# Performance work log

Measured on AMD Instinct MI355X. Metric: run time of the kernel, lower is better.

The kernel has to match this reference:

```python
import jax, jax.numpy as jnp
import numpy as np

B, S, H, NH = 1, 4096, 768, 12
D = H // NH  # per-head dim = 64


def setup_inputs() -> dict:
    key = jax.random.key(0)
    ks = jax.random.split(key, 10)
    p = 0.02  # param scale
    return {
        "x": jax.random.normal(ks[0], (B, S, H), jnp.float32),
        "Wq": jax.random.normal(ks[1], (H, H), jnp.float32) * p,
        "bq": jax.random.normal(ks[2], (H,), jnp.float32) * p,
        "Wk": jax.random.normal(ks[3], (H, H), jnp.float32) * p,
        "bk": jax.random.normal(ks[4], (H,), jnp.float32) * p,
        "Wv": jax.random.normal(ks[5], (H, H), jnp.float32) * p,
        "bv": jax.random.normal(ks[6], (H,), jnp.float32) * p,
        "Wo": jax.random.normal(ks[7], (H, H), jnp.float32) * p,
        "bo": jax.random.normal(ks[8], (H,), jnp.float32) * p,
        "attn_mask": jax.random.randint(ks[9], (B, 1, 1, S), 0, 2).astype(bool),
    }


def _split_heads(t):
    # [B, S, H] -> [B, NH, S, D]
    return t.reshape(B, S, NH, D).transpose(0, 2, 1, 3)


def reference(x, Wq, bq, Wk, bk, Wv, bv, Wo, bo, attn_mask):
    q = _split_heads(x @ Wq.T + bq)
    k = _split_heads(x @ Wk.T + bk)
    v = _split_heads(x @ Wv.T + bv)
    scores = jnp.einsum('bhqd,bhkd->bhqk', q, k) / np.sqrt(D).astype(np.float32)
    scores = jnp.where(attn_mask, jnp.float32(-1e9), scores)
    attn = jax.nn.softmax(scores, axis=-1)
    ctx = jnp.einsum('bhqk,bhkd->bhqd', attn, v)
    ctx = ctx.transpose(0, 2, 1, 3).reshape(B, S, H)  # merge heads
    return ctx @ Wo.T + bo
```

## Files before the change

kernel.cpp:

```cpp
#include <hip/hip_runtime.h>
#include <stdint.h>

#define S_LEN 4096
#define HDIM  768
#define NHEAD 12
#define DHEAD 64

typedef _Float16 f16;
typedef __attribute__((ext_vector_type(8))) _Float16 f16x8;
typedef __attribute__((ext_vector_type(4))) _Float16 f16x4;
typedef __attribute__((ext_vector_type(4))) float   f32x4;

typedef __attribute__((address_space(1))) void gv_t;
typedef __attribute__((address_space(3))) void lv_t;

__device__ __forceinline__ void async_copy16(const void* g, void* l) {
  __builtin_amdgcn_global_load_lds((gv_t*)g, (lv_t*)l, 16, 0, 0);
}

__device__ __forceinline__ float fast_exp2(float x) {
#if __has_builtin(__builtin_amdgcn_exp2f)
  return __builtin_amdgcn_exp2f(x);
#else
  return exp2f(x);
#endif
}

__device__ __forceinline__ int swz4(int row) { return (row ^ (row >> 2)) & 3; }

constexpr size_t OFF_META = 0;
constexpr size_t OFF_POS  = 256;
constexpr size_t OFF_XB   = 65536;
constexpr size_t SZ_XB    = (size_t)S_LEN * HDIM * 2;
constexpr size_t OFF_WQKV = OFF_XB + SZ_XB;
constexpr size_t SZ_WQKV  = (size_t)3 * HDIM * HDIM * 2;
constexpr size_t OFF_WO   = OFF_WQKV + SZ_WQKV;
constexpr size_t SZ_WO    = (size_t)HDIM * HDIM * 2;
constexpr size_t OFF_Q    = OFF_WO + SZ_WO;
constexpr size_t SZ_HD    = (size_t)NHEAD * S_LEN * DHEAD * 2;
constexpr size_t OFF_K    = OFF_Q + SZ_HD;
constexpr size_t OFF_VT   = OFF_K + SZ_HD;
constexpr size_t OFF_CTX  = OFF_VT + SZ_HD;
constexpr size_t SZ_CTX   = (size_t)S_LEN * HDIM * 2;
constexpr size_t OFF_PO   = OFF_CTX + SZ_CTX;
constexpr size_t SZ_PO    = (size_t)2 * NHEAD * S_LEN * DHEAD * 2;
constexpr size_t OFF_PL   = OFF_PO + SZ_PO;

__global__ __launch_bounds__(256) void k_cvt5(const float* __restrict__ x,
                                              const float* __restrict__ wq,
                                              const float* __restrict__ wk,
                                              const float* __restrict__ wv,
                                              const float* __restrict__ wo,
                                              f16* __restrict__ dst) {
  int i = blockIdx.x * 256 + threadIdx.x;
  const float* src; int off;
  if (i < 786432) { src = x; off = i; }
  else {
    int j = i - 786432;
    int w = j / 147456;
    off = j - w * 147456;
    src = (w == 0) ? wq : (w == 1) ? wk : (w == 2) ? wv : wo;
  }
  float4 v = ((const float4*)src)[off];
  f16x4 h;
  h[0] = (f16)v.x; h[1] = (f16)v.y; h[2] = (f16)v.z; h[3] = (f16)v.w;
  ((f16x4*)dst)[i] = h;
}

__global__ __launch_bounds__(1024) void k_mask(const int* __restrict__ mi,
                                               int* __restrict__ pos,
                                               int* __restrict__ meta) {
  __shared__ int s_flag;
  __shared__ int s_cnt[1024];
  const int tid = threadIdx.x;
  if (tid == 0) s_flag = 1;
  __syncthreads();
  int v = mi[tid];
  if (v != 0 && v != 1) atomicAnd(&s_flag, 0);
  __syncthreads();
  const int isInt = s_flag;
  const unsigned char* mu8 = (const unsigned char*)mi;
  int keep[4]; int cnt = 0;
  #pragma unroll
  for (int k = 0; k < 4; ++k) {
    int s = tid * 4 + k;
    int mval = isInt ? mi[s] : (int)mu8[s];
    keep[k] = (mval == 0) ? 1 : 0;
    cnt += keep[k];
  }
  s_cnt[tid] = cnt;
  __syncthreads();
  for (int off = 1; off < 1024; off <<= 1) {
    int t = (tid >= off) ? s_cnt[tid - off] : 0;
    __syncthreads();
    s_cnt[tid] += t;
    __syncthreads();
  }
  int base = s_cnt[tid] - cnt;
  #pragma unroll
  for (int k = 0; k < 4; ++k) {
    int s = tid * 4 + k;
    pos[s] = keep[k] ? base : -1;
    base += keep[k];
  }
  if (tid == 1023) meta[0] = s_cnt[1023];
}

__global__ __launch_bounds__(256) void k_pad(const int* __restrict__ meta,
                                             f16* __restrict__ Kc, f16* __restrict__ Vtc) {
  const int kc = meta[0];
  const int kcp = (kc + 63) & ~63;
  const int npad = kcp - kc;
  if (npad == 0) return;
  const int h = blockIdx.x, tid = threadIdx.x;
  for (int idx = tid; idx < 64 * 64; idx += 256) {
    int r = idx >> 6, d = idx & 63;
    if (r < npad) Kc[((size_t)h * S_LEN + kc + r) * DHEAD + d] = (f16)0.f;
  }
  for (int idx = tid; idx < 64 * 64; idx += 256) {
    int d = idx >> 6, c = idx & 63;
    if (c < npad) Vtc[((size_t)h * DHEAD + d) * S_LEN + kc + c] = (f16)0.f;
  }
}

__global__ __launch_bounds__(256) void k_qkv(
    const f16* __restrict__ xb, const f16* __restrict__ wqkv,
    const float* __restrict__ bq, const float* __restrict__ bk, const float* __restrict__ bv,
    const int* __restrict__ pos,
    f16* __restrict__ Qh, f16* __restrict__ Kc, f16* __restrict__ Vtc) {
  __shared__ __attribute__((aligned(16))) f16 lA[128 * 32];
  __shared__ __attribute__((aligned(16))) f16 lB[128 * 32];
  const int tid = threadIdx.x;
  const int wid = tid >> 6, lane = tid & 63;
  const int quad = lane >> 4, l16 = lane & 15;
  const int wm = wid >> 1, wn = wid & 1;
  const int tn = blockIdx.x;
  const int m0 = blockIdx.y * 128;
  const int mat = tn / 6;
  const int nb = (tn % 6) * 128;
  const f16* wbase = wqkv + (size_t)mat * HDIM * HDIM;

  f32x4 acc[4][4] = {};

  for (int k0 = 0; k0 < HDIM; k0 += 32) {
    #pragma unroll
    for (int iss = 0; iss < 2; ++iss) {
      int c = iss * 256 + tid;
      int row = c >> 2, slot = c & 3;
      int gs = slot ^ swz4(row);
      async_copy16((const char*)(xb + (size_t)(m0 + row) * HDIM + k0) + gs * 16,
                   (char*)lA + (iss * 256 + wid * 64) * 16);
      async_copy16((const char*)(wbase + (size_t)(nb + row) * HDIM + k0) + gs * 16,
                   (char*)lB + (iss * 256 + wid * 64) * 16);
    }
    __syncthreads();
    f16x8 af[4], bf[4];
    #pragma unroll
    for (int mi = 0; mi < 4; ++mi) {
      int row = wm * 64 + mi * 16 + l16;
      af[mi] = *(const f16x8*)&lA[row * 32 + (quad ^ swz4(row)) * 8];
    }
    #pragma unroll
    for (int ni = 0; ni < 4; ++ni) {
      int row = wn * 64 + ni * 16 + l16;
      bf[ni] = *(const f16x8*)&lB[row * 32 + (quad ^ swz4(row)) * 8];
    }
    #pragma unroll
    for (int mi = 0; mi < 4; ++mi)
      #pragma unroll
      for (int ni = 0; ni < 4; ++ni)
        acc[mi][ni] = __builtin_amdgcn_mfma_f32_16x16x32_f16(af[mi], bf[ni], acc[mi][ni], 0, 0, 0);
    __syncthreads();
  }

  const float* bias = (mat == 0) ? bq : (mat == 1) ? bk : bv;
  const float qscale = 0.125f * 1.44269504088896341f;
  #pragma unroll
  for (int mi = 0; mi < 4; ++mi) {
    int srow = m0 + wm * 64 + mi * 16 + quad * 4;
    #pragma unroll
    for (int ni = 0; ni < 4; ++ni) {
      int n = nb + wn * 64 + ni * 16 + l16;
      int head = n >> 6, d = n & 63;
      float b = bias[n];
      #pragma unroll
      for (int r = 0; r < 4; ++r) {
        int s = srow + r;
        float val = acc[mi][ni][r] + b;
        if (mat == 0) {
          Qh[((size_t)head * S_LEN + s) * DHEAD + d] = (f16)(val * qscale);
        } else {
          int p = pos[s];
          if (p >= 0) {
            if (mat == 1) Kc[((size_t)head * S_LEN + p) * DHEAD + d] = (f16)val;
            else          Vtc[((size_t)head * DHEAD + d) * S_LEN + p] = (f16)val;
          }
        }
      }
    }
  }
}

__global__ __launch_bounds__(256) void k_attn(
    const f16* __restrict__ Qh, const f16* __restrict__ Kc, const f16* __restrict__ Vtc,
    const int* __restrict__ meta, f16* __restrict__ PO, float* __restrict__ PL) {
  __shared__ __attribute__((aligned(16))) f16 lK[64 * 64];
  __shared__ __attribute__((aligned(16))) f16 lV[64 * 64];
  __shared__ __attribute__((aligned(16))) f16 lP[4][16 * 64];
  const int tid = threadIdx.x;
  const int wid = tid >> 6, lane = tid & 63;
  const int quad = lane >> 4, l16 = lane & 15;
  const int head = blockIdx.y;
  const int q0 = blockIdx.x * 64;
  const int split = blockIdx.z;
  const int kc = meta[0];
  const int nkt = (kc + 63) >> 6;
  const int th = nkt >> 1;
  const int t0 = split ? th : 0;
  const int t1 = split ? nkt : th;
  const float npad = split ? (float)(nkt * 64 - kc) : 0.f;

  const f16* Qp = Qh + ((size_t)head * S_LEN + q0 + wid * 16 + l16) * DHEAD;
  f16x8 qf0 = *(const f16x8*)(Qp + quad * 8);
  f16x8 qf1 = *(const f16x8*)(Qp + 32 + quad * 8);

  f16x8 onesb;
  #pragma unroll
  for (int i = 0; i < 8; ++i) onesb[i] = (f16)1.0f;

  f32x4 accO[4] = {};
  f32x4 lacc = {};

  const char* kbase = (const char*)(Kc + (size_t)head * S_LEN * DHEAD);
  const char* vbase = (const char*)(Vtc + (size_t)head * DHEAD * S_LEN);

  for (int it = t0; it < t1; ++it) {
    const int j0 = it * 64;
    #pragma unroll
    for (int iss = 0; iss < 2; ++iss) {
      int c = iss * 256 + tid;
      int row = c >> 3, slot = c & 7;
      int gs = slot ^ (row & 7);
      async_copy16(kbase + (size_t)(j0 + row) * 128 + gs * 16,
                   (char*)lK + (iss * 256 + wid * 64) * 16);
      async_copy16(vbase + (size_t)row * (S_LEN * 2) + (size_t)j0 * 2 + gs * 16,
                   (char*)lV + (iss * 256 + wid * 64) * 16);
    }
    __syncthreads();

    f32x4 sacc[4] = {};
    #pragma unroll
    for (int kt = 0; kt < 2; ++kt) {
      f16x8 q = kt ? qf1 : qf0;
      #pragma unroll
      for (int ni = 0; ni < 4; ++ni) {
        int key = ni * 16 + l16;
        int slot = (kt * 4 + quad) ^ (key & 7);
        f16x8 b = *(const f16x8*)&lK[key * 64 + slot * 8];
        sacc[ni] = __builtin_amdgcn_mfma_f32_16x16x32_f16(q, b, sacc[ni], 0, 0, 0);
      }
    }

    #pragma unroll
    for (int ni = 0; ni < 4; ++ni)
      #pragma unroll
      for (int r = 0; r < 4; ++r)
        sacc[ni][r] = fast_exp2(sacc[ni][r]);

    f16* pw = &lP[wid][0];
    #pragma unroll
    for (int ni = 0; ni < 4; ++ni) {
      int col = ni * 16 + l16;
      #pragma unroll
      for (int r = 0; r < 4; ++r) {
        int rr = quad * 4 + r;
        int slot = (col >> 3) ^ (rr & 7);
        pw[rr * 64 + slot * 8 + (col & 7)] = (f16)sacc[ni][r];
      }
    }
    #pragma unroll
    for (int kt = 0; kt < 2; ++kt) {
      int slotp = (kt * 4 + quad) ^ (l16 & 7);
      f16x8 pf = *(const f16x8*)&pw[l16 * 64 + slotp * 8];
      lacc = __builtin_amdgcn_mfma_f32_16x16x32_f16(pf, onesb, lacc, 0, 0, 0);
      #pragma unroll
      for (int nd = 0; nd < 4; ++nd) {
        int d = nd * 16 + l16;
        int slotv = (kt * 4 + quad) ^ (d & 7);
        f16x8 b = *(const f16x8*)&lV[d * 64 + slotv * 8];
        accO[nd] = __builtin_amdgcn_mfma_f32_16x16x32_f16(pf, b, accO[nd], 0, 0, 0);
      }
    }
    __syncthreads();
  }

  if (l16 == 0) {
    #pragma unroll
    for (int r = 0; r < 4; ++r)
      PL[((size_t)split * NHEAD + head) * S_LEN + q0 + wid * 16 + quad * 4 + r] =
          lacc[r] - npad;
  }
  #pragma unroll
  for (int nd = 0; nd < 4; ++nd) {
    #pragma unroll
    for (int r = 0; r < 4; ++r) {
      int s = q0 + wid * 16 + quad * 4 + r;
      PO[(((size_t)split * NHEAD + head) * S_LEN + s) * DHEAD + nd * 16 + l16] =
          (f16)accO[nd][r];
    }
  }
}

__global__ __launch_bounds__(256) void k_comb(const f16* __restrict__ PO,
                                              const float* __restrict__ PL,
                                              f16* __restrict__ ctx) {
  int u = blockIdx.x * 256 + threadIdx.x;
  int s = u / 96;
  int c = u - s * 96;
  int h = c >> 3, db = (c & 7) * 8;
  size_t i0 = ((size_t)h * S_LEN + s) * DHEAD + db;
  size_t i1 = ((size_t)(NHEAD + h) * S_LEN + s) * DHEAD + db;
  f16x8 o0 = *(const f16x8*)(PO + i0);
  f16x8 o1 = *(const f16x8*)(PO + i1);
  float l = PL[(size_t)h * S_LEN + s] + PL[(size_t)(NHEAD + h) * S_LEN + s];
  float inv = 1.0f / l;
  f16x8 o;
  #pragma unroll
  for (int i = 0; i < 8; ++i) o[i] = (f16)(((float)o0[i] + (float)o1[i]) * inv);
  *(f16x8*)(ctx + (size_t)s * HDIM + h * DHEAD + db) = o;
}

__global__ __launch_bounds__(256) void k_out(
    const f16* __restrict__ ctx, const f16* __restrict__ wo,
    const float* __restrict__ bo, float* __restrict__ out) {
  __shared__ __attribute__((aligned(16))) f16 lA[128 * 32];
  __shared__ __attribute__((aligned(16))) f16 lB[128 * 32];
  const int tid = threadIdx.x;
  const int wid = tid >> 6, lane = tid & 63;
  const int quad = lane >> 4, l16 = lane & 15;
  const int wm = wid >> 1, wn = wid & 1;
  const int nb = blockIdx.x * 128;
  const int m0 = blockIdx.y * 128;

  f32x4 acc[4][4] = {};

  for (int k0 = 0; k0 < HDIM; k0 += 32) {
    #pragma unroll
    for (int iss = 0; iss < 2; ++iss) {
      int c = iss * 256 + tid;
      int row = c >> 2, slot = c & 3;
      int gs = slot ^ swz4(row);
      async_copy16((const char*)(ctx + (size_t)(m0 + row) * HDIM + k0) + gs * 16,
                   (char*)lA + (iss * 256 + wid * 64) * 16);
      async_copy16((const char*)(wo + (size_t)(nb + row) * HDIM + k0) + gs * 16,
                   (char*)lB + (iss * 256 + wid * 64) * 16);
    }
    __syncthreads();
    f16x8 af[4], bf[4];
    #pragma unroll
    for (int mi = 0; mi < 4; ++mi) {
      int row = wm * 64 + mi * 16 + l16;
      af[mi] = *(const f16x8*)&lA[row * 32 + (quad ^ swz4(row)) * 8];
    }
    #pragma unroll
    for (int ni = 0; ni < 4; ++ni) {
      int row = wn * 64 + ni * 16 + l16;
      bf[ni] = *(const f16x8*)&lB[row * 32 + (quad ^ swz4(row)) * 8];
    }
    #pragma unroll
    for (int mi = 0; mi < 4; ++mi)
      #pragma unroll
      for (int ni = 0; ni < 4; ++ni)
        acc[mi][ni] = __builtin_amdgcn_mfma_f32_16x16x32_f16(af[mi], bf[ni], acc[mi][ni], 0, 0, 0);
    __syncthreads();
  }

  #pragma unroll
  for (int mi = 0; mi < 4; ++mi) {
    int srow = m0 + wm * 64 + mi * 16 + quad * 4;
    #pragma unroll
    for (int ni = 0; ni < 4; ++ni) {
      int n = nb + wn * 64 + ni * 16 + l16;
      float b = bo[n];
      #pragma unroll
      for (int r = 0; r < 4; ++r)
        out[(size_t)(srow + r) * HDIM + n] = acc[mi][ni][r] + b;
    }
  }
}

extern "C" void kernel_launch(void* const* d_in, const int* in_sizes, int n_in,
                              void* d_out, int out_size, void* d_ws, size_t ws_size,
                              hipStream_t stream) {
  const float* x  = (const float*)d_in[0];
  const float* Wq = (const float*)d_in[1];
  const float* bq = (const float*)d_in[2];
  const float* Wk = (const float*)d_in[3];
  const float* bk = (const float*)d_in[4];
  const float* Wv = (const float*)d_in[5];
  const float* bv = (const float*)d_in[6];
  const float* Wo = (const float*)d_in[7];
  const float* bo = (const float*)d_in[8];
  const int*   mask = (const int*)d_in[9];
  float* out = (float*)d_out;

  char* ws = (char*)d_ws;
  int* meta = (int*)(ws + OFF_META);
  int* pos  = (int*)(ws + OFF_POS);
  f16* xb   = (f16*)(ws + OFF_XB);
  f16* wqkv = (f16*)(ws + OFF_WQKV);
  f16* wob  = (f16*)(ws + OFF_WO);
  f16* Qh   = (f16*)(ws + OFF_Q);
  f16* Kc   = (f16*)(ws + OFF_K);
  f16* Vtc  = (f16*)(ws + OFF_VT);
  f16* ctx  = (f16*)(ws + OFF_CTX);
  f16* PO   = (f16*)(ws + OFF_PO);
  float* PL = (float*)(ws + OFF_PL);

  k_cvt5<<<dim3(5376), 256, 0, stream>>>(x, Wq, Wk, Wv, Wo, xb);
  k_mask<<<dim3(1), 1024, 0, stream>>>(mask, pos, meta);
  k_qkv<<<dim3(18, 32), 256, 0, stream>>>(xb, wqkv, bq, bk, bv, pos, Qh, Kc, Vtc);
  k_pad<<<dim3(NHEAD), 256, 0, stream>>>(meta, Kc, Vtc);
  k_attn<<<dim3(64, NHEAD, 2), 256, 0, stream>>>(Qh, Kc, Vtc, meta, PO, PL);
  k_comb<<<dim3((S_LEN * 96) / 256), 256, 0, stream>>>(PO, PL, ctx);
  k_out<<<dim3(6, 32), 256, 0, stream>>>(ctx, wob, bo, out);
}
```

Measured before the change: 208.2 us.

## Switch attention to 32x32 MFMA, stage V transpose, fuse prep kernels

Rewrites the attention inner loop around 32x32x16 MFMA tiles, with 32 queries per wave and 128 queries per block. The row sum is now accumulated in registers instead of through a ones-vector MFMA. V is written row-major by the QKV GEMM and then transposed through LDS by a new kernel, which replaces the scattered strided transposed stores. Fp32-to-fp16 conversion, K zeroing and mask compaction are merged into one prep launch, and the separate pad kernel is removed. Workspace regions are aliased to reuse memory, which relies on strict kernel ordering and adds a full zero-fill of K.

```diff
diff --git a/kernel.cpp b/kernel.cpp
--- a/kernel.cpp
+++ b/kernel.cpp
@@ -7,9 +7,10 @@
 #define DHEAD 64
 
 typedef _Float16 f16;
-typedef __attribute__((ext_vector_type(8))) _Float16 f16x8;
-typedef __attribute__((ext_vector_type(4))) _Float16 f16x4;
-typedef __attribute__((ext_vector_type(4))) float   f32x4;
+typedef __attribute__((ext_vector_type(8)))  _Float16 f16x8;
+typedef __attribute__((ext_vector_type(4)))  _Float16 f16x4;
+typedef __attribute__((ext_vector_type(4)))  float    f32x4;
+typedef __attribute__((ext_vector_type(16))) float    f32x16;
 
 typedef __attribute__((address_space(1))) void gv_t;
 typedef __attribute__((address_space(3))) void lv_t;
@@ -40,57 +41,68 @@
 constexpr size_t SZ_HD    = (size_t)NHEAD * S_LEN * DHEAD * 2;
 constexpr size_t OFF_K    = OFF_Q + SZ_HD;
 constexpr size_t OFF_VT   = OFF_K + SZ_HD;
-constexpr size_t OFF_CTX  = OFF_VT + SZ_HD;
-constexpr size_t SZ_CTX   = (size_t)S_LEN * HDIM * 2;
-constexpr size_t OFF_PO   = OFF_CTX + SZ_CTX;
-constexpr size_t SZ_PO    = (size_t)2 * NHEAD * S_LEN * DHEAD * 2;
-constexpr size_t OFF_PL   = OFF_PO + SZ_PO;
-
-__global__ __launch_bounds__(256) void k_cvt5(const float* __restrict__ x,
+constexpr size_t OFF_VR   = OFF_VT + SZ_HD;
+constexpr size_t OFF_PO1  = OFF_VR + SZ_HD;
+
+__global__ __launch_bounds__(256) void k_prep(const float* __restrict__ x,
                                               const float* __restrict__ wq,
                                               const float* __restrict__ wk,
                                               const float* __restrict__ wv,
                                               const float* __restrict__ wo,
-                                              f16* __restrict__ dst) {
-  int i = blockIdx.x * 256 + threadIdx.x;
-  const float* src; int off;
-  if (i < 786432) { src = x; off = i; }
-  else {
-    int j = i - 786432;
-    int w = j / 147456;
-    off = j - w * 147456;
-    src = (w == 0) ? wq : (w == 1) ? wk : (w == 2) ? wv : wo;
-  }
-  float4 v = ((const float4*)src)[off];
-  f16x4 h;
-  h[0] = (f16)v.x; h[1] = (f16)v.y; h[2] = (f16)v.z; h[3] = (f16)v.w;
-  ((f16x4*)dst)[i] = h;
-}
-
-__global__ __launch_bounds__(1024) void k_mask(const int* __restrict__ mi,
-                                               int* __restrict__ pos,
-                                               int* __restrict__ meta) {
+                                              const int* __restrict__ mi,
+                                              f16* __restrict__ dst,
+                                              f16* __restrict__ Kc,
+                                              int* __restrict__ pos,
+                                              int* __restrict__ meta) {
   __shared__ int s_flag;
-  __shared__ int s_cnt[1024];
-  const int tid = threadIdx.x;
+  __shared__ int s_cnt[256];
+  const int b = blockIdx.x, tid = threadIdx.x;
+  if (b < 5376) {
+    int i = b * 256 + tid;
+    const float* src; int off;
+    if (i < 786432) { src = x; off = i; }
+    else {
+      int j = i - 786432;
+      int w = j / 147456;
+      off = j - w * 147456;
+      src = (w == 0) ? wq : (w == 1) ? wk : (w == 2) ? wv : wo;
+    }
+    float4 v = ((const float4*)src)[off];
+    f16x4 h;
+    h[0] = (f16)v.x; h[1] = (f16)v.y; h[2] = (f16)v.z; h[3] = (f16)v.w;
+    ((f16x4*)dst)[i] = h;
+    return;
+  }
+  if (b < 6144) {
+    int u = (b - 5376) * 512 + tid;
+    f16x8 z = {};
+    ((f16x8*)Kc)[u] = z;
+    ((f16x8*)Kc)[u + 256] = z;
+    return;
+  }
   if (tid == 0) s_flag = 1;
   __syncthreads();
-  int v = mi[tid];
-  if (v != 0 && v != 1) atomicAnd(&s_flag, 0);
+  int bad = 0;
+  #pragma unroll
+  for (int k = 0; k < 4; ++k) {
+    int v = mi[k * 256 + tid];
+    if (v != 0 && v != 1) bad = 1;
+  }
+  if (bad) atomicAnd(&s_flag, 0);
   __syncthreads();
   const int isInt = s_flag;
   const unsigned char* mu8 = (const unsigned char*)mi;
-  int keep[4]; int cnt = 0;
-  #pragma unroll
-  for (int k = 0; k < 4; ++k) {
-    int s = tid * 4 + k;
-    int mval = isInt ? mi[s] : (int)mu8[s];
+  int keep[16]; int cnt = 0;
+  const int s0 = tid * 16;
+  #pragma unroll
+  for (int k = 0; k < 16; ++k) {
+    int mval = isInt ? mi[s0 + k] : (int)mu8[s0 + k];
     keep[k] = (mval == 0) ? 1 : 0;
     cnt += keep[k];
   }
   s_cnt[tid] = cnt;
   __syncthreads();
-  for (int off = 1; off < 1024; off <<= 1) {
+  for (int off = 1; off < 256; off <<= 1) {
     int t = (tid >= off) ? s_cnt[tid - off] : 0;
     __syncthreads();
     s_cnt[tid] += t;
@@ -98,36 +110,18 @@
   }
   int base = s_cnt[tid] - cnt;
   #pragma unroll
-  for (int k = 0; k < 4; ++k) {
-    int s = tid * 4 + k;
-    pos[s] = keep[k] ? base : -1;
+  for (int k = 0; k < 16; ++k) {
+    pos[s0 + k] = keep[k] ? base : -1;
     base += keep[k];
   }
-  if (tid == 1023) meta[0] = s_cnt[1023];
-}
-
-__global__ __launch_bounds__(256) void k_pad(const int* __restrict__ meta,
-                                             f16* __restrict__ Kc, f16* __restrict__ Vtc) {
-  const int kc = meta[0];
-  const int kcp = (kc + 63) & ~63;
-  const int npad = kcp - kc;
-  if (npad == 0) return;
-  const int h = blockIdx.x, tid = threadIdx.x;
-  for (int idx = tid; idx < 64 * 64; idx += 256) {
-    int r = idx >> 6, d = idx & 63;
-    if (r < npad) Kc[((size_t)h * S_LEN + kc + r) * DHEAD + d] = (f16)0.f;
-  }
-  for (int idx = tid; idx < 64 * 64; idx += 256) {
-    int d = idx >> 6, c = idx & 63;
-    if (c < npad) Vtc[((size_t)h * DHEAD + d) * S_LEN + kc + c] = (f16)0.f;
-  }
+  if (tid == 255) meta[0] = s_cnt[255];
 }
 
 __global__ __launch_bounds__(256) void k_qkv(
     const f16* __restrict__ xb, const f16* __restrict__ wqkv,
     const float* __restrict__ bq, const float* __restrict__ bk, const float* __restrict__ bv,
     const int* __restrict__ pos,
-    f16* __restrict__ Qh, f16* __restrict__ Kc, f16* __restrict__ Vtc) {
+    f16* __restrict__ Qh, f16* __restrict__ Kc, f16* __restrict__ Vrow) {
   __shared__ __attribute__((aligned(16))) f16 lA[128 * 32];
   __shared__ __attribute__((aligned(16))) f16 lB[128 * 32];
   const int tid = threadIdx.x;
@@ -175,6 +169,7 @@
 
   const float* bias = (mat == 0) ? bq : (mat == 1) ? bk : bv;
   const float qscale = 0.125f * 1.44269504088896341f;
+  f16* kvdst = (mat == 1) ? Kc : Vrow;
   #pragma unroll
   for (int mi = 0; mi < 4; ++mi) {
     int srow = m0 + wm * 64 + mi * 16 + quad * 4;
@@ -191,48 +186,70 @@
           Qh[((size_t)head * S_LEN + s) * DHEAD + d] = (f16)(val * qscale);
         } else {
           int p = pos[s];
-          if (p >= 0) {
-            if (mat == 1) Kc[((size_t)head * S_LEN + p) * DHEAD + d] = (f16)val;
-            else          Vtc[((size_t)head * DHEAD + d) * S_LEN + p] = (f16)val;
-          }
+          if (p >= 0)
+            kvdst[((size_t)head * S_LEN + p) * DHEAD + d] = (f16)val;
         }
       }
     }
   }
 }
 
+__global__ __launch_bounds__(256) void k_vt(const int* __restrict__ meta,
+                                            const f16* __restrict__ Vrow,
+                                            f16* __restrict__ Vtc) {
+  const int kc = meta[0];
+  const int kcp = (kc + 63) & ~63;
+  const int p0 = blockIdx.x * 64;
+  const int h = blockIdx.y;
+  if (p0 >= kcp) return;
+  __shared__ __attribute__((aligned(16))) f16 lT[64 * 80];
+  const int tid = threadIdx.x;
+  for (int u = tid; u < 512; u += 256) {
+    int d8 = u >> 6, p = u & 63;
+    f16x8 v = {};
+    if (p0 + p < kc) v = *(const f16x8*)&Vrow[((size_t)h * S_LEN + p0 + p) * DHEAD + d8 * 8];
+    #pragma unroll
+    for (int j = 0; j < 8; ++j) lT[(d8 * 8 + j) * 80 + p] = v[j];
+  }
+  __syncthreads();
+  for (int w = tid; w < 512; w += 256) {
+    int d = w >> 3, p8 = w & 7;
+    f16x8 o = *(const f16x8*)&lT[d * 80 + p8 * 8];
+    *(f16x8*)&Vtc[((size_t)h * DHEAD + d) * S_LEN + p0 + p8 * 8] = o;
+  }
+}
+
 __global__ __launch_bounds__(256) void k_attn(
     const f16* __restrict__ Qh, const f16* __restrict__ Kc, const f16* __restrict__ Vtc,
-    const int* __restrict__ meta, f16* __restrict__ PO, float* __restrict__ PL) {
+    const int* __restrict__ meta, f16* __restrict__ PO0, f16* __restrict__ PO1,
+    float* __restrict__ PL) {
   __shared__ __attribute__((aligned(16))) f16 lK[64 * 64];
   __shared__ __attribute__((aligned(16))) f16 lV[64 * 64];
-  __shared__ __attribute__((aligned(16))) f16 lP[4][16 * 64];
+  __shared__ __attribute__((aligned(16))) f16 lP[4][32 * 64];
   const int tid = threadIdx.x;
   const int wid = tid >> 6, lane = tid & 63;
-  const int quad = lane >> 4, l16 = lane & 15;
+  const int hf = lane >> 5, q = lane & 31, r7 = q & 7;
   const int head = blockIdx.y;
-  const int q0 = blockIdx.x * 64;
+  const int q0 = blockIdx.x * 128 + wid * 32;
   const int split = blockIdx.z;
   const int kc = meta[0];
   const int nkt = (kc + 63) >> 6;
   const int th = nkt >> 1;
   const int t0 = split ? th : 0;
   const int t1 = split ? nkt : th;
-  const float npad = split ? (float)(nkt * 64 - kc) : 0.f;
-
-  const f16* Qp = Qh + ((size_t)head * S_LEN + q0 + wid * 16 + l16) * DHEAD;
-  f16x8 qf0 = *(const f16x8*)(Qp + quad * 8);
-  f16x8 qf1 = *(const f16x8*)(Qp + 32 + quad * 8);
-
-  f16x8 onesb;
-  #pragma unroll
-  for (int i = 0; i < 8; ++i) onesb[i] = (f16)1.0f;
-
-  f32x4 accO[4] = {};
-  f32x4 lacc = {};
+  const float npadf = split ? (float)(nkt * 64 - kc) : 0.f;
+
+  const f16* Qp = Qh + ((size_t)head * S_LEN + q0 + q) * DHEAD;
+  f16x8 qf[4];
+  #pragma unroll
+  for (int t = 0; t < 4; ++t) qf[t] = *(const f16x8*)(Qp + t * 16 + hf * 8);
+
+  f32x16 accO0 = {}, accO1 = {};
+  float lsum = 0.f;
 
   const char* kbase = (const char*)(Kc + (size_t)head * S_LEN * DHEAD);
   const char* vbase = (const char*)(Vtc + (size_t)head * DHEAD * S_LEN);
+  f16* pw = &lP[wid][0];
 
   for (int it = t0; it < t1; ++it) {
     const int j0 = it * 64;
@@ -248,70 +265,58 @@
     }
     __syncthreads();
 
-    f32x4 sacc[4] = {};
-    #pragma unroll
-    for (int kt = 0; kt < 2; ++kt) {
-      f16x8 q = kt ? qf1 : qf0;
+    f32x16 sA = {}, sB = {};
+    #pragma unroll
+    for (int t = 0; t < 4; ++t) {
+      int so = ((2 * t + hf) ^ r7) * 8;
+      f16x8 a0 = *(const f16x8*)&lK[q * 64 + so];
+      f16x8 a1 = *(const f16x8*)&lK[(32 + q) * 64 + so];
+      sA = __builtin_amdgcn_mfma_f32_32x32x16_f16(a0, qf[t], sA, 0, 0, 0);
+      sB = __builtin_amdgcn_mfma_f32_32x32x16_f16(a1, qf[t], sB, 0, 0, 0);
+    }
+
+    #pragma unroll
+    for (int i = 0; i < 16; ++i) { sA[i] = fast_exp2(sA[i]); lsum += sA[i]; }
+    #pragma unroll
+    for (int i = 0; i < 16; ++i) { sB[i] = fast_exp2(sB[i]); lsum += sB[i]; }
+
+    #pragma unroll
+    for (int g = 0; g < 4; ++g) {
+      f16x4 w0, w1;
       #pragma unroll
-      for (int ni = 0; ni < 4; ++ni) {
-        int key = ni * 16 + l16;
-        int slot = (kt * 4 + quad) ^ (key & 7);
-        f16x8 b = *(const f16x8*)&lK[key * 64 + slot * 8];
-        sacc[ni] = __builtin_amdgcn_mfma_f32_16x16x32_f16(q, b, sacc[ni], 0, 0, 0);
-      }
-    }
-
-    #pragma unroll
-    for (int ni = 0; ni < 4; ++ni)
-      #pragma unroll
-      for (int r = 0; r < 4; ++r)
-        sacc[ni][r] = fast_exp2(sacc[ni][r]);
-
-    f16* pw = &lP[wid][0];
-    #pragma unroll
-    for (int ni = 0; ni < 4; ++ni) {
-      int col = ni * 16 + l16;
-      #pragma unroll
-      for (int r = 0; r < 4; ++r) {
-        int rr = quad * 4 + r;
-        int slot = (col >> 3) ^ (rr & 7);
-        pw[rr * 64 + slot * 8 + (col & 7)] = (f16)sacc[ni][r];
-      }
-    }
-    #pragma unroll
-    for (int kt = 0; kt < 2; ++kt) {
-      int slotp = (kt * 4 + quad) ^ (l16 & 7);
-      f16x8 pf = *(const f16x8*)&pw[l16 * 64 + slotp * 8];
-      lacc = __builtin_amdgcn_mfma_f32_16x16x32_f16(pf, onesb, lacc, 0, 0, 0);
-      #pragma unroll
-      for (int nd = 0; nd < 4; ++nd) {
-        int d = nd * 16 + l16;
-        int slotv = (kt * 4 + quad) ^ (d & 7);
-        f16x8 b = *(const f16x8*)&lV[d * 64 + slotv * 8];
-        accO[nd] = __builtin_amdgcn_mfma_f32_16x16x32_f16(pf, b, accO[nd], 0, 0, 0);
-      }
-    }
-    __syncthreads();
-  }
-
-  if (l16 == 0) {
-    #pragma unroll
-    for (int r = 0; r < 4; ++r)
-      PL[((size_t)split * NHEAD + head) * S_LEN + q0 + wid * 16 + quad * 4 + r] =
-          lacc[r] - npad;
-  }
-  #pragma unroll
-  for (int nd = 0; nd < 4; ++nd) {
-    #pragma unroll
-    for (int r = 0; r < 4; ++r) {
-      int s = q0 + wid * 16 + quad * 4 + r;
-      PO[(((size_t)split * NHEAD + head) * S_LEN + s) * DHEAD + nd * 16 + l16] =
-          (f16)accO[nd][r];
-    }
-  }
-}
-
-__global__ __launch_bounds__(256) void k_comb(const f16* __restrict__ PO,
+      for (int r = 0; r < 4; ++r) { w0[r] = (f16)sA[4 * g + r]; w1[r] = (f16)sB[4 * g + r]; }
+      *(f16x4*)&pw[q * 64 + (g ^ r7) * 8 + hf * 4]       = w0;
+      *(f16x4*)&pw[q * 64 + ((4 + g) ^ r7) * 8 + hf * 4] = w1;
+    }
+
+    #pragma unroll
+    for (int t = 0; t < 4; ++t) {
+      int so = ((2 * t + hf) ^ r7) * 8;
+      f16x8 pf = *(const f16x8*)&pw[q * 64 + so];
+      f16x8 v0 = *(const f16x8*)&lV[q * 64 + so];
+      f16x8 v1 = *(const f16x8*)&lV[(32 + q) * 64 + so];
+      accO0 = __builtin_amdgcn_mfma_f32_32x32x16_f16(pf, v0, accO0, 0, 0, 0);
+      accO1 = __builtin_amdgcn_mfma_f32_32x32x16_f16(pf, v1, accO1, 0, 0, 0);
+    }
+    __syncthreads();
+  }
+
+  lsum += __shfl_xor(lsum, 32, 64);
+  lsum -= npadf;
+  if (hf == 0)
+    PL[((size_t)split * NHEAD + head) * S_LEN + q0 + q] = lsum;
+
+  f16* PO = split ? PO1 : PO0;
+  #pragma unroll
+  for (int reg = 0; reg < 16; ++reg) {
+    int s = q0 + (reg & 3) + 8 * (reg >> 2) + 4 * hf;
+    PO[((size_t)head * S_LEN + s) * DHEAD + q]      = (f16)accO0[reg];
+    PO[((size_t)head * S_LEN + s) * DHEAD + 32 + q] = (f16)accO1[reg];
+  }
+}
+
+__global__ __launch_bounds__(256) void k_comb(const f16* __restrict__ PO0,
+                                              const f16* __restrict__ PO1,
                                               const float* __restrict__ PL,
                                               f16* __restrict__ ctx) {
   int u = blockIdx.x * 256 + threadIdx.x;
@@ -319,9 +324,8 @@
   int c = u - s * 96;
   int h = c >> 3, db = (c & 7) * 8;
   size_t i0 = ((size_t)h * S_LEN + s) * DHEAD + db;
-  size_t i1 = ((size_t)(NHEAD + h) * S_LEN + s) * DHEAD + db;
-  f16x8 o0 = *(const f16x8*)(PO + i0);
-  f16x8 o1 = *(const f16x8*)(PO + i1);
+  f16x8 o0 = *(const f16x8*)(PO0 + i0);
+  f16x8 o1 = *(const f16x8*)(PO1 + i0);
   float l = PL[(size_t)h * S_LEN + s] + PL[(size_t)(NHEAD + h) * S_LEN + s];
   float inv = 1.0f / l;
   f16x8 o;
@@ -405,23 +409,24 @@
   float* out = (float*)d_out;
 
   char* ws = (char*)d_ws;
-  int* meta = (int*)(ws + OFF_META);
-  int* pos  = (int*)(ws + OFF_POS);
-  f16* xb   = (f16*)(ws + OFF_XB);
-  f16* wqkv = (f16*)(ws + OFF_WQKV);
-  f16* wob  = (f16*)(ws + OFF_WO);
-  f16* Qh   = (f16*)(ws + OFF_Q);
-  f16* Kc   = (f16*)(ws + OFF_K);
-  f16* Vtc  = (f16*)(ws + OFF_VT);
-  f16* ctx  = (f16*)(ws + OFF_CTX);
-  f16* PO   = (f16*)(ws + OFF_PO);
-  float* PL = (float*)(ws + OFF_PL);
-
-  k_cvt5<<<dim3(5376), 256, 0, stream>>>(x, Wq, Wk, Wv, Wo, xb);
-  k_mask<<<dim3(1), 1024, 0, stream>>>(mask, pos, meta);
-  k_qkv<<<dim3(18, 32), 256, 0, stream>>>(xb, wqkv, bq, bk, bv, pos, Qh, Kc, Vtc);
-  k_pad<<<dim3(NHEAD), 256, 0, stream>>>(meta, Kc, Vtc);
-  k_attn<<<dim3(64, NHEAD, 2), 256, 0, stream>>>(Qh, Kc, Vtc, meta, PO, PL);
-  k_comb<<<dim3((S_LEN * 96) / 256), 256, 0, stream>>>(PO, PL, ctx);
+  int* meta  = (int*)(ws + OFF_META);
+  int* pos   = (int*)(ws + OFF_POS);
+  f16* xb    = (f16*)(ws + OFF_XB);
+  f16* wqkv  = (f16*)(ws + OFF_WQKV);
+  f16* wob   = (f16*)(ws + OFF_WO);
+  f16* Qh    = (f16*)(ws + OFF_Q);
+  f16* Kc    = (f16*)(ws + OFF_K);
+  f16* Vtc   = (f16*)(ws + OFF_VT);
+  f16* Vrow  = (f16*)(ws + OFF_VR);
+  f16* PO0   = (f16*)(ws + OFF_VR);
+  f16* PO1   = (f16*)(ws + OFF_PO1);
+  float* PL  = (float*)(ws + OFF_WQKV);
+  f16* ctx   = (f16*)(ws + OFF_XB);
+
+  k_prep<<<dim3(6145), 256, 0, stream>>>(x, Wq, Wk, Wv, Wo, mask, xb, Kc, pos, meta);
+  k_qkv<<<dim3(18, 32), 256, 0, stream>>>(xb, wqkv, bq, bk, bv, pos, Qh, Kc, Vrow);
+  k_vt<<<dim3(64, NHEAD), 256, 0, stream>>>(meta, Vrow, Vtc);
+  k_attn<<<dim3(32, NHEAD, 2), 256, 0, stream>>>(Qh, Kc, Vtc, meta, PO0, PO1, PL);
+  k_comb<<<dim3((S_LEN * 96) / 256), 256, 0, stream>>>(PO0, PO1, PL, ctx);
   k_out<<<dim3(6, 32), 256, 0, stream>>>(ctx, wob, bo, out);
 }
```

Measured after the change: 192.4 us. 7.6% less time.
